# Kernel optimization log

Hardware: AMD Instinct MI355X
Metric: run time of the kernel (lower is better)

Reference implementation:

```python
import jax, jax.numpy as jnp
import numpy as np

V, E, H, L, T_BLOCK = 50257, 1024, 16, 8, 1024
HS = E // H  # 64
F_ = 4 * E
STD = 0.02


def _ln(x, g, b, eps=1e-5):
    mu = jnp.mean(x, axis=-1, keepdims=True)
    var = jnp.var(x, axis=-1, keepdims=True)
    return (x - mu) * jax.lax.rsqrt(var + eps) * g + b


def setup_inputs() -> dict:
    key = jax.random.key(0)
    ks = jax.random.split(key, 16)
    n = lambda k, shp: (STD * jax.random.normal(k, shp)).astype(jnp.float32)
    inp = {
        "idx": jax.random.randint(ks[0], (4, 1024), 0, V, dtype=jnp.int32).astype(jnp.int64),
        "tok_emb": n(ks[1], (V, E)),
        "pos_emb": n(ks[2], (T_BLOCK, E)),
        "wq": n(ks[3], (L, H, E, HS)),
        "wk": n(ks[4], (L, H, E, HS)),
        "wv": n(ks[5], (L, H, E, HS)),
        "wo": n(ks[6], (L, E, E)),
        "bo": jnp.zeros((L, E), jnp.float32),
        "ln1g": jnp.ones((L, E), jnp.float32),
        "ln1b": jnp.zeros((L, E), jnp.float32),
        "ln2g": jnp.ones((L, E), jnp.float32),
        "ln2b": jnp.zeros((L, E), jnp.float32),
        "w1": n(ks[7], (L, E, F_)),
        "b1": jnp.zeros((L, F_), jnp.float32),
        "w2": n(ks[8], (L, F_, E)),
        "b2": jnp.zeros((L, E), jnp.float32),
        "lnfg": jnp.ones((E,), jnp.float32),
        "lnfb": jnp.zeros((E,), jnp.float32),
    }
    return inp


def reference(idx, tok_emb, pos_emb, wq, wk, wv, wo, bo, ln1g, ln1b,
              ln2g, ln2b, w1, b1, w2, b2, lnfg, lnfb):
    B, T = idx.shape
    x = tok_emb[idx] + pos_emb[:T]  # [B,T,E]
    mask = jnp.tril(jnp.ones((T, T), dtype=bool))  # causal
    scale = HS ** -0.5
    for l in range(L):
        h = _ln(x, ln1g[l], ln1b[l])
        q = jnp.einsum('bte,hed->bhtd', h, wq[l])
        k = jnp.einsum('bte,hed->bhtd', h, wk[l])
        v = jnp.einsum('bte,hed->bhtd', h, wv[l])
        att = jnp.einsum('bhtd,bhsd->bhts', q, k) * scale
        att = jnp.where(mask, att, -jnp.inf)
        att = jax.nn.softmax(att, axis=-1)
        o = jnp.einsum('bhts,bhsd->bhtd', att, v)
        o = o.transpose(0, 2, 1, 3).reshape(B, T, E)  # concat heads
        x = x + o @ wo[l] + bo[l]
        h2 = _ln(x, ln2g[l], ln2b[l])
        x = x + jax.nn.relu(h2 @ w1[l] + b1[l]) @ w2[l] + b2[l]
    x = _ln(x, lnfg, lnfb)
    logits = x @ tok_emb.T  # tied lm_head, no bias
    return logits
```

## Files before the change

kernel.cpp:

```cpp
#include <hip/hip_runtime.h>
#include <cstdint>

#define B_ 4
#define T_ 1024
#define E_ 1024
#define H_ 16
#define HS_ 64
#define L_ 8
#define F_DIM 4096
#define V_ 50257
#define VP_ 50304

typedef __attribute__((ext_vector_type(8))) short bf16x8;
typedef __attribute__((ext_vector_type(4))) float f32x4;
typedef unsigned short u16;

__device__ inline float b2f(u16 u) {
  unsigned int v = ((unsigned int)u) << 16;
  return __builtin_bit_cast(float, v);
}
__device__ inline u16 f2b(float f) {
  unsigned int u = __builtin_bit_cast(unsigned int, f);
  unsigned int r = (u + 0x7FFFu + ((u >> 16) & 1u)) >> 16;
  return (u16)r;
}

__device__ inline float wave_sum(float v) {
#pragma unroll
  for (int off = 32; off > 0; off >>= 1) v += __shfl_down(v, off);
  return v;
}

#define GLOAD16(gp, lp)                                                        \
  __builtin_amdgcn_global_load_lds(                                            \
      (const __attribute__((address_space(1))) unsigned int*)(gp),             \
      (__attribute__((address_space(3))) unsigned int*)(lp), 16, 0, 0)

__global__ __launch_bounds__(256) void embed_kernel(
    const int* __restrict__ idx, const float* __restrict__ tok,
    const float* __restrict__ pos, float* __restrict__ x) {
  int bt = blockIdx.x;
  int t = bt & (T_ - 1);
  int tid = threadIdx.x;
  int tokid = idx[bt];
  float4 a = reinterpret_cast<const float4*>(tok + (size_t)tokid * E_)[tid];
  float4 p = reinterpret_cast<const float4*>(pos + (size_t)t * E_)[tid];
  float4 r = make_float4(a.x + p.x, a.y + p.y, a.z + p.z, a.w + p.w);
  reinterpret_cast<float4*>(x + (size_t)bt * E_)[tid] = r;
}

__global__ __launch_bounds__(256) void ln_kernel(
    const float* __restrict__ in, const float* __restrict__ g,
    const float* __restrict__ b, u16* __restrict__ out) {
  int row = blockIdx.x;
  int tid = threadIdx.x;
  const float* xr = in + (size_t)row * E_;
  float4 v = reinterpret_cast<const float4*>(xr)[tid];
  float s = v.x + v.y + v.z + v.w;
  float q = v.x * v.x + v.y * v.y + v.z * v.z + v.w * v.w;
  s = wave_sum(s);
  q = wave_sum(q);
  __shared__ float ls[4], lq[4];
  int wid = tid >> 6;
  if ((tid & 63) == 0) { ls[wid] = s; lq[wid] = q; }
  __syncthreads();
  float st = ls[0] + ls[1] + ls[2] + ls[3];
  float qt = lq[0] + lq[1] + lq[2] + lq[3];
  float mu = st * (1.0f / E_);
  float var = qt * (1.0f / E_) - mu * mu;
  float inv = rsqrtf(var + 1e-5f);
  float4 gg = reinterpret_cast<const float4*>(g)[tid];
  float4 bb = reinterpret_cast<const float4*>(b)[tid];
  ushort4 o4;
  o4.x = f2b((v.x - mu) * inv * gg.x + bb.x);
  o4.y = f2b((v.y - mu) * inv * gg.y + bb.y);
  o4.z = f2b((v.z - mu) * inv * gg.z + bb.z);
  o4.w = f2b((v.w - mu) * inv * gg.w + bb.w);
  reinterpret_cast<ushort4*>(out + (size_t)row * E_)[tid] = o4;
}

__global__ __launch_bounds__(256) void convT_kernel(
    const float* __restrict__ in, u16* __restrict__ out, int K, int N) {
  __shared__ float tile[64][65];
  int n0 = blockIdx.x * 64, k0 = blockIdx.y * 64;
  int tx = threadIdx.x & 63, ty = threadIdx.x >> 6;
#pragma unroll
  for (int r = 0; r < 64; r += 4)
    tile[r + ty][tx] = in[(size_t)(k0 + r + ty) * N + n0 + tx];
  __syncthreads();
#pragma unroll
  for (int r = 0; r < 64; r += 4)
    out[(size_t)(n0 + r + ty) * K + k0 + tx] = f2b(tile[tx][r + ty]);
}

__global__ __launch_bounds__(256) void convQKV_kernel(
    const float* __restrict__ wq, const float* __restrict__ wk,
    const float* __restrict__ wv, u16* __restrict__ out) {
  int src = blockIdx.x >> 4, hh = blockIdx.x & 15, e0 = blockIdx.y * 64;
  const float* w =
      (src == 0 ? wq : (src == 1 ? wk : wv)) + (size_t)hh * E_ * HS_;
  __shared__ float tile[64][65];
  int tx = threadIdx.x & 63, ty = threadIdx.x >> 6;
#pragma unroll
  for (int r = 0; r < 64; r += 4)
    tile[r + ty][tx] = w[(size_t)(e0 + r + ty) * HS_ + tx];
  __syncthreads();
  size_t nb = (size_t)src * 1024 + hh * 64;
#pragma unroll
  for (int r = 0; r < 64; r += 4)
    out[(nb + r + ty) * E_ + e0 + tx] = f2b(tile[tx][r + ty]);
}

__global__ __launch_bounds__(256) void convTok_kernel(
    const float* __restrict__ tok, u16* __restrict__ out) {
  int row = blockIdx.x;
  int tid = threadIdx.x;
  ushort4 o4;
  if (row < V_) {
    float4 v = reinterpret_cast<const float4*>(tok + (size_t)row * E_)[tid];
    o4.x = f2b(v.x); o4.y = f2b(v.y); o4.z = f2b(v.z); o4.w = f2b(v.w);
  } else {
    o4 = make_ushort4(0, 0, 0, 0);
  }
  reinterpret_cast<ushort4*>(out + (size_t)row * E_)[tid] = o4;
}

__global__ __launch_bounds__(256) void vtrans_kernel(
    const u16* __restrict__ qkv, u16* __restrict__ vt) {
  int t0 = blockIdx.x * 64;
  int bh = blockIdx.y;
  int b = bh >> 4, hh = bh & 15;
  __shared__ unsigned int tile[64][65];
  int tx = threadIdx.x & 63, ty = threadIdx.x >> 6;
  const u16* src = qkv + ((size_t)(b * T_ + t0)) * 3072 + 2048 + hh * 64;
#pragma unroll
  for (int r = 0; r < 64; r += 4)
    tile[r + ty][tx] = src[(size_t)(r + ty) * 3072 + tx];
  __syncthreads();
  u16* dst = vt + ((size_t)bh * 64) * 1024 + t0;
#pragma unroll
  for (int r = 0; r < 64; r += 4)
    dst[(size_t)(r + ty) * 1024 + tx] = (u16)tile[tx][r + ty];
}

__global__ __launch_bounds__(256) void mfma_gemm_kernel(
    const u16* __restrict__ A, int lda, const u16* __restrict__ Bt, int ldb,
    const float* __restrict__ bias, float* __restrict__ Cf,
    u16* __restrict__ Cb, int ldc, int N, int K, int flags) {
  __shared__ u16 As[128 * 32];
  __shared__ u16 Bs[128 * 32];
  int m0 = blockIdx.x * 128, n0 = blockIdx.y * 128;
  int tid = threadIdx.x;
  int wave = tid >> 6, lane = tid & 63;
  int wr = wave >> 1, wc = wave & 1;

  f32x4 acc[4][4];
#pragma unroll
  for (int i = 0; i < 4; ++i)
#pragma unroll
    for (int j = 0; j < 4; ++j) acc[i][j] = (f32x4){0.f, 0.f, 0.f, 0.f};

  int c0 = wave * 2, c1 = wave * 2 + 1;
  int sr0 = c0 * 16 + (lane >> 2), sr1 = c1 * 16 + (lane >> 2);
  int sc = (lane & 3) * 8;
  const u16* Ag0 = A + (size_t)(m0 + sr0) * lda + sc;
  const u16* Ag1 = A + (size_t)(m0 + sr1) * lda + sc;
  const u16* Bg0 = Bt + (size_t)(n0 + sr0) * ldb + sc;
  const u16* Bg1 = Bt + (size_t)(n0 + sr1) * ldb + sc;
  u16* lA0 = &As[c0 * 512];
  u16* lA1 = &As[c1 * 512];
  u16* lB0 = &Bs[c0 * 512];
  u16* lB1 = &Bs[c1 * 512];

  int lrow = lane & 15, loct = lane >> 4;
  const int arow0 = (wr * 64 + lrow) * 32 + loct * 8;
  const int brow0 = (wc * 64 + lrow) * 32 + loct * 8;

  for (int k0 = 0; k0 < K; k0 += 32) {
    GLOAD16(Ag0 + k0, lA0);
    GLOAD16(Ag1 + k0, lA1);
    GLOAD16(Bg0 + k0, lB0);
    GLOAD16(Bg1 + k0, lB1);
    __syncthreads();
    bf16x8 af[4], bfr[4];
#pragma unroll
    for (int mf = 0; mf < 4; ++mf)
      af[mf] = *(const bf16x8*)&As[arow0 + mf * 16 * 32];
#pragma unroll
    for (int nf = 0; nf < 4; ++nf)
      bfr[nf] = *(const bf16x8*)&Bs[brow0 + nf * 16 * 32];
#pragma unroll
    for (int mf = 0; mf < 4; ++mf)
#pragma unroll
      for (int nf = 0; nf < 4; ++nf)
        acc[mf][nf] = __builtin_amdgcn_mfma_f32_16x16x32_bf16(
            af[mf], bfr[nf], acc[mf][nf], 0, 0, 0);
    __syncthreads();
  }

  int lq = lane >> 4;
#pragma unroll
  for (int mf = 0; mf < 4; ++mf) {
#pragma unroll
    for (int nf = 0; nf < 4; ++nf) {
      int n = n0 + wc * 64 + nf * 16 + lrow;
      if (n < N) {
        float bv = bias ? bias[n] : 0.f;
#pragma unroll
        for (int j = 0; j < 4; ++j) {
          int m = m0 + wr * 64 + mf * 16 + lq * 4 + j;
          float r = acc[mf][nf][j] + bv;
          if (flags & 1) r += Cf[(size_t)m * ldc + n];
          if (flags & 2) r = fmaxf(r, 0.f);
          if (Cb)
            Cb[(size_t)m * ldc + n] = f2b(r);
          else
            Cf[(size_t)m * ldc + n] = r;
        }
      }
    }
  }
}

__global__ __launch_bounds__(256) void fattn_kernel(
    const u16* __restrict__ qkv, const u16* __restrict__ vt,
    u16* __restrict__ o) {
  int t0 = (gridDim.x - 1 - blockIdx.x) * 64;
  int bh = blockIdx.y;
  int b = bh >> 4, hh = bh & 15;
  int tid = threadIdx.x;
  int w = tid >> 6, lane = tid & 63;
  int c = lane & 15, g = lane >> 4;

  __shared__ u16 Ks[64][72];
  __shared__ u16 Vs[64][72];
  __shared__ u16 Ps[4][16][72];

  const u16* qbase = qkv + (size_t)(b * T_) * 3072 + hh * 64;
  const u16* kbase = qbase + 1024;
  const u16* vbase = vt + (size_t)bh * 64 * 1024;

  bf16x8 qf[2];
  {
    const u16* qrow = qbase + (size_t)(t0 + w * 16 + c) * 3072 + g * 8;
#pragma unroll
    for (int kh = 0; kh < 2; ++kh) {
      bf16x8 tq = *(const bf16x8*)(qrow + kh * 32);
#pragma unroll
      for (int j = 0; j < 8; ++j) tq[j] = (short)f2b(b2f((u16)tq[j]) * 0.125f);
      qf[kh] = tq;
    }
  }

  float m[4] = {-1e30f, -1e30f, -1e30f, -1e30f};
  float l[4] = {0.f, 0.f, 0.f, 0.f};
  f32x4 acc[4];
#pragma unroll
  for (int ds = 0; ds < 4; ++ds) acc[ds] = (f32x4){0.f, 0.f, 0.f, 0.f};

  int tq0 = t0 + w * 16 + g * 4;

  for (int kv0 = 0; kv0 <= t0; kv0 += 64) {
    __syncthreads();
#pragma unroll
    for (int i = tid; i < 512; i += 256) {
      int r = i >> 3, cc = i & 7;
      *(int4*)&Ks[r][cc * 8] =
          *(const int4*)(kbase + (size_t)(kv0 + r) * 3072 + cc * 8);
      *(int4*)&Vs[r][cc * 8] =
          *(const int4*)(vbase + (size_t)r * 1024 + kv0 + cc * 8);
    }
    __syncthreads();

    f32x4 s[4];
#pragma unroll
    for (int ct = 0; ct < 4; ++ct) {
      bf16x8 kf0 = *(const bf16x8*)&Ks[ct * 16 + c][g * 8];
      bf16x8 kf1 = *(const bf16x8*)&Ks[ct * 16 + c][g * 8 + 32];
      s[ct] = (f32x4){0.f, 0.f, 0.f, 0.f};
      s[ct] =
          __builtin_amdgcn_mfma_f32_16x16x32_bf16(qf[0], kf0, s[ct], 0, 0, 0);
      s[ct] =
          __builtin_amdgcn_mfma_f32_16x16x32_bf16(qf[1], kf1, s[ct], 0, 0, 0);
    }
#pragma unroll
    for (int ct = 0; ct < 4; ++ct) {
      int tk = kv0 + ct * 16 + c;
#pragma unroll
      for (int j = 0; j < 4; ++j)
        if (tk > tq0 + j) s[ct][j] = -1e30f;
    }
#pragma unroll
    for (int j = 0; j < 4; ++j) {
      float mt = fmaxf(fmaxf(s[0][j], s[1][j]), fmaxf(s[2][j], s[3][j]));
#pragma unroll
      for (int off = 1; off < 16; off <<= 1)
        mt = fmaxf(mt, __shfl_xor(mt, off));
      float mn = fmaxf(m[j], mt);
      float sc = __expf(m[j] - mn);
      m[j] = mn;
      float rs = 0.f;
#pragma unroll
      for (int ct = 0; ct < 4; ++ct) {
        float p = __expf(s[ct][j] - mn);
        s[ct][j] = p;
        rs += p;
      }
#pragma unroll
      for (int off = 1; off < 16; off <<= 1) rs += __shfl_xor(rs, off);
      l[j] = l[j] * sc + rs;
#pragma unroll
      for (int ds = 0; ds < 4; ++ds) acc[ds][j] *= sc;
    }
#pragma unroll
    for (int ct = 0; ct < 4; ++ct)
#pragma unroll
      for (int j = 0; j < 4; ++j)
        Ps[w][g * 4 + j][ct * 16 + c] = f2b(s[ct][j]);
    bf16x8 pf0 = *(const bf16x8*)&Ps[w][c][g * 8];
    bf16x8 pf1 = *(const bf16x8*)&Ps[w][c][g * 8 + 32];
#pragma unroll
    for (int ds = 0; ds < 4; ++ds) {
      bf16x8 vf0 = *(const bf16x8*)&Vs[ds * 16 + c][g * 8];
      bf16x8 vf1 = *(const bf16x8*)&Vs[ds * 16 + c][g * 8 + 32];
      acc[ds] =
          __builtin_amdgcn_mfma_f32_16x16x32_bf16(pf0, vf0, acc[ds], 0, 0, 0);
      acc[ds] =
          __builtin_amdgcn_mfma_f32_16x16x32_bf16(pf1, vf1, acc[ds], 0, 0, 0);
    }
  }

  float inv[4];
#pragma unroll
  for (int j = 0; j < 4; ++j) inv[j] = 1.0f / l[j];
  u16* orow = o + ((size_t)(b * T_ + tq0)) * E_ + hh * 64;
#pragma unroll
  for (int ds = 0; ds < 4; ++ds)
#pragma unroll
    for (int j = 0; j < 4; ++j)
      orow[(size_t)j * E_ + ds * 16 + c] = f2b(acc[ds][j] * inv[j]);
}

extern "C" void kernel_launch(void* const* d_in, const int* in_sizes, int n_in,
                              void* d_out, int out_size, void* d_ws,
                              size_t ws_size, hipStream_t stream) {
  (void)in_sizes; (void)n_in; (void)out_size; (void)ws_size;
  const int* idx = (const int*)d_in[0];
  const float* tok_emb = (const float*)d_in[1];
  const float* pos_emb = (const float*)d_in[2];
  const float* wq = (const float*)d_in[3];
  const float* wk = (const float*)d_in[4];
  const float* wv = (const float*)d_in[5];
  const float* wo = (const float*)d_in[6];
  const float* bo = (const float*)d_in[7];
  const float* ln1g = (const float*)d_in[8];
  const float* ln1b = (const float*)d_in[9];
  const float* ln2g = (const float*)d_in[10];
  const float* ln2b = (const float*)d_in[11];
  const float* w1 = (const float*)d_in[12];
  const float* b1 = (const float*)d_in[13];
  const float* w2 = (const float*)d_in[14];
  const float* b2 = (const float*)d_in[15];
  const float* lnfg = (const float*)d_in[16];
  const float* lnfb = (const float*)d_in[17];
  float* out = (float*)d_out;
  char* ws = (char*)d_ws;

  u16* h = (u16*)(ws + 0);
  float* x = (float*)(ws + 8388608);
  u16* qkvb = (u16*)(ws + 25165824);
  u16* ob = (u16*)(ws + 50331648);
  u16* ffb = (u16*)(ws + 58720256);
  u16* wqkvT = (u16*)(ws + 92274688);
  u16* woT = (u16*)(ws + 98566144);
  u16* w1T = (u16*)(ws + 100663296);
  u16* w2T = (u16*)(ws + 109051904);
  u16* vtb = (u16*)(ws + 117440512);
  u16* tokb = (u16*)(ws + 8388608);

  embed_kernel<<<B_ * T_, 256, 0, stream>>>(idx, tok_emb, pos_emb, x);

  for (int l = 0; l < L_; ++l) {
    ln_kernel<<<B_ * T_, 256, 0, stream>>>(x, ln1g + l * E_, ln1b + l * E_, h);
    convQKV_kernel<<<dim3(48, 16), 256, 0, stream>>>(
        wq + (size_t)l * H_ * E_ * HS_, wk + (size_t)l * H_ * E_ * HS_,
        wv + (size_t)l * H_ * E_ * HS_, wqkvT);
    mfma_gemm_kernel<<<dim3(32, 24), 256, 0, stream>>>(
        h, E_, wqkvT, E_, nullptr, nullptr, qkvb, 3072, 3072, E_, 0);
    vtrans_kernel<<<dim3(16, 64), 256, 0, stream>>>(qkvb, vtb);
    fattn_kernel<<<dim3(16, 64), 256, 0, stream>>>(qkvb, vtb, ob);
    convT_kernel<<<dim3(16, 16), 256, 0, stream>>>(
        wo + (size_t)l * E_ * E_, woT, E_, E_);
    mfma_gemm_kernel<<<dim3(32, 8), 256, 0, stream>>>(
        ob, E_, woT, E_, bo + (size_t)l * E_, x, nullptr, E_, E_, E_, 1);
    ln_kernel<<<B_ * T_, 256, 0, stream>>>(x, ln2g + l * E_, ln2b + l * E_, h);
    convT_kernel<<<dim3(64, 16), 256, 0, stream>>>(
        w1 + (size_t)l * E_ * F_DIM, w1T, E_, F_DIM);
    mfma_gemm_kernel<<<dim3(32, 32), 256, 0, stream>>>(
        h, E_, w1T, E_, b1 + (size_t)l * F_DIM, nullptr, ffb, F_DIM, F_DIM,
        E_, 2);
    convT_kernel<<<dim3(16, 64), 256, 0, stream>>>(
        w2 + (size_t)l * F_DIM * E_, w2T, F_DIM, E_);
    mfma_gemm_kernel<<<dim3(32, 8), 256, 0, stream>>>(
        ffb, F_DIM, w2T, F_DIM, b2 + (size_t)l * E_, x, nullptr, E_, E_,
        F_DIM, 1);
  }

  ln_kernel<<<B_ * T_, 256, 0, stream>>>(x, lnfg, lnfb, h);
  convTok_kernel<<<VP_, 256, 0, stream>>>(tok_emb, tokb);
  mfma_gemm_kernel<<<dim3(32, VP_ / 128), 256, 0, stream>>>(
      h, E_, tokb, E_, nullptr, out, nullptr, V_, V_, E_, 0);
}
```

Before: 3.641 ms.

## Add 256x256 double-buffered MFMA GEMM with XCD-aware block remap

Adds a new 512-thread GEMM kernel that uses 256x256 output tiles and 64-wide K steps. Operands are staged in double-buffered, XOR-swizzled LDS through direct global-to-LDS loads, and each next-tile prefetch is interleaved with the current tile's MFMA work under explicit waitcnt and barrier control. Workgroup IDs are remapped so consecutive tiles land on the same XCD, which should improve L2 reuse. The QKV, FFN-up and lm_head GEMMs switch to this kernel, with vocab padding raised to a multiple of 256. This raises LDS use to 128KB per block and lowers occupancy, and the convTok workspace now holds more padded rows.

Measured after the change: 3.324 ms. -8.7%, faster.

```diff
diff --git a/kernel.cpp b/kernel.cpp
--- a/kernel.cpp
+++ b/kernel.cpp
@@ -9,7 +9,7 @@
 #define L_ 8
 #define F_DIM 4096
 #define V_ 50257
-#define VP_ 50304
+#define VP2_ 50432
 
 typedef __attribute__((ext_vector_type(8))) short bf16x8;
 typedef __attribute__((ext_vector_type(4))) float f32x4;
@@ -143,6 +143,145 @@
     dst[(size_t)(r + ty) * 1024 + tx] = (u16)tile[tx][r + ty];
 }
 
+__global__ __launch_bounds__(512) void gemm8p_kernel(
+    const u16* __restrict__ A, int lda, const u16* __restrict__ Bt, int ldb,
+    const float* __restrict__ bias, float* __restrict__ Cf,
+    u16* __restrict__ Cb, int ldc, int N, int K, int gn, int flags) {
+  __shared__ u16 As[2][256 * 64];
+  __shared__ u16 Bs[2][256 * 64];
+
+  int nwg = gridDim.x;
+  int q8 = nwg >> 3;
+  int bid = blockIdx.x;
+  int wg = (bid & 7) * q8 + (bid >> 3);
+  int m0 = (wg / gn) * 256, n0 = (wg % gn) * 256;
+
+  int tid = threadIdx.x;
+  int w = tid >> 6, lane = tid & 63;
+  int wr = w >> 2, wc = w & 3;
+  int l15 = lane & 15, lg = lane >> 4;
+  int swzr = (l15 & 7) << 3;
+
+  int l8 = lane >> 3;
+  int swz_e = ((lane & 7) ^ l8) << 3;
+  int wq = w & 3, wh = w >> 2;
+  const u16* aSrc[4];
+  const u16* bSrc[4];
+#pragma unroll
+  for (int qq = 0; qq < 4; ++qq) {
+    aSrc[qq] = A + (size_t)(m0 + wh * 128 + qq * 32 + wq * 8 + l8) * lda;
+    bSrc[qq] = Bt + (size_t)(n0 + (w >> 1) * 64 + qq * 16 + (w & 1) * 8 + l8) * ldb;
+  }
+
+#define STAGE_A(qq, tt, bb)                                                    \
+  GLOAD16(aSrc[qq] + (size_t)(tt) * 64 + swz_e,                                \
+          &As[bb][(wh * 128 + (qq) * 32 + wq * 8) * 64])
+#define STAGE_B(qq, tt, bb)                                                    \
+  GLOAD16(bSrc[qq] + (size_t)(tt) * 64 + swz_e,                                \
+          &Bs[bb][((w >> 1) * 64 + (qq) * 16 + (w & 1) * 8) * 64])
+#define LDA_OFF(mf, ks) \
+  (((wr * 128 + (mf) * 16 + l15) * 64) + ((((ks) * 32) + lg * 8) ^ swzr))
+#define LDB_OFF(nf, ks) \
+  (((wc * 64 + (nf) * 16 + l15) * 64) + ((((ks) * 32) + lg * 8) ^ swzr))
+#define WAITV(n) asm volatile("s_waitcnt vmcnt(" #n ")" ::: "memory")
+
+  f32x4 acc[8][4];
+#pragma unroll
+  for (int i = 0; i < 8; ++i)
+#pragma unroll
+    for (int j = 0; j < 4; ++j) acc[i][j] = (f32x4){0.f, 0.f, 0.f, 0.f};
+
+  STAGE_B(0, 0, 0); STAGE_B(1, 0, 0); STAGE_B(2, 0, 0); STAGE_B(3, 0, 0);
+  STAGE_A(0, 0, 0); STAGE_A(1, 0, 0); STAGE_A(2, 0, 0); STAGE_A(3, 0, 0);
+  WAITV(3);
+  __builtin_amdgcn_sched_barrier(0);
+  __builtin_amdgcn_s_barrier();
+  __builtin_amdgcn_sched_barrier(0);
+
+  int NT = K >> 6;
+  bf16x8 bfrag[4][2];
+  for (int t = 0; t < NT; ++t) {
+    int cur = t & 1, nxt = cur ^ 1;
+    bool pf = (t + 1 < NT);
+    int t1 = t + 1;
+#pragma unroll
+    for (int p = 0; p < 4; ++p) {
+      bf16x8 a0k0 = *(const bf16x8*)&As[cur][LDA_OFF(2 * p + 0, 0)];
+      bf16x8 a0k1 = *(const bf16x8*)&As[cur][LDA_OFF(2 * p + 0, 1)];
+      bf16x8 a1k0 = *(const bf16x8*)&As[cur][LDA_OFF(2 * p + 1, 0)];
+      bf16x8 a1k1 = *(const bf16x8*)&As[cur][LDA_OFF(2 * p + 1, 1)];
+      if (p == 0) {
+#pragma unroll
+        for (int nf = 0; nf < 4; ++nf) {
+          bfrag[nf][0] = *(const bf16x8*)&Bs[cur][LDB_OFF(nf, 0)];
+          bfrag[nf][1] = *(const bf16x8*)&Bs[cur][LDB_OFF(nf, 1)];
+        }
+      }
+      if (pf) {
+        if (p == 0) { STAGE_B(0, t1, nxt); STAGE_B(1, t1, nxt); }
+        else if (p == 1) { STAGE_B(2, t1, nxt); STAGE_B(3, t1, nxt); }
+        else if (p == 2) { STAGE_A(0, t1, nxt); STAGE_A(1, t1, nxt); }
+        else { STAGE_A(2, t1, nxt); STAGE_A(3, t1, nxt); }
+      }
+      __builtin_amdgcn_s_barrier();
+      asm volatile("s_waitcnt lgkmcnt(0)" ::: "memory");
+      __builtin_amdgcn_sched_barrier(0);
+      __builtin_amdgcn_s_setprio(1);
+#pragma unroll
+      for (int nf = 0; nf < 4; ++nf) {
+        acc[2 * p + 0][nf] = __builtin_amdgcn_mfma_f32_16x16x32_bf16(
+            a0k0, bfrag[nf][0], acc[2 * p + 0][nf], 0, 0, 0);
+        acc[2 * p + 0][nf] = __builtin_amdgcn_mfma_f32_16x16x32_bf16(
+            a0k1, bfrag[nf][1], acc[2 * p + 0][nf], 0, 0, 0);
+        acc[2 * p + 1][nf] = __builtin_amdgcn_mfma_f32_16x16x32_bf16(
+            a1k0, bfrag[nf][0], acc[2 * p + 1][nf], 0, 0, 0);
+        acc[2 * p + 1][nf] = __builtin_amdgcn_mfma_f32_16x16x32_bf16(
+            a1k1, bfrag[nf][1], acc[2 * p + 1][nf], 0, 0, 0);
+      }
+      __builtin_amdgcn_s_setprio(0);
+      if (pf) {
+        if (p == 0) WAITV(4);
+        else if (p == 1) WAITV(5);
+        else if (p == 2) WAITV(6);
+        else WAITV(3);
+      } else {
+        if (p == 0) WAITV(2);
+        else if (p == 1) WAITV(1);
+        else WAITV(0);
+      }
+      __builtin_amdgcn_sched_barrier(0);
+      __builtin_amdgcn_s_barrier();
+      __builtin_amdgcn_sched_barrier(0);
+    }
+  }
+
+#pragma unroll
+  for (int mf = 0; mf < 8; ++mf) {
+#pragma unroll
+    for (int nf = 0; nf < 4; ++nf) {
+      int n = n0 + wc * 64 + nf * 16 + l15;
+      if (n < N) {
+        float bv = bias ? bias[n] : 0.f;
+#pragma unroll
+        for (int j = 0; j < 4; ++j) {
+          int m = m0 + wr * 128 + mf * 16 + lg * 4 + j;
+          float r = acc[mf][nf][j] + bv;
+          if (flags & 2) r = fmaxf(r, 0.f);
+          if (Cb)
+            Cb[(size_t)m * ldc + n] = f2b(r);
+          else
+            Cf[(size_t)m * ldc + n] = r;
+        }
+      }
+    }
+  }
+#undef STAGE_A
+#undef STAGE_B
+#undef LDA_OFF
+#undef LDB_OFF
+#undef WAITV
+}
+
 __global__ __launch_bounds__(256) void mfma_gemm_kernel(
     const u16* __restrict__ A, int lda, const u16* __restrict__ Bt, int ldb,
     const float* __restrict__ bias, float* __restrict__ Cf,
@@ -385,8 +524,8 @@
     convQKV_kernel<<<dim3(48, 16), 256, 0, stream>>>(
         wq + (size_t)l * H_ * E_ * HS_, wk + (size_t)l * H_ * E_ * HS_,
         wv + (size_t)l * H_ * E_ * HS_, wqkvT);
-    mfma_gemm_kernel<<<dim3(32, 24), 256, 0, stream>>>(
-        h, E_, wqkvT, E_, nullptr, nullptr, qkvb, 3072, 3072, E_, 0);
+    gemm8p_kernel<<<16 * 12, 512, 0, stream>>>(
+        h, E_, wqkvT, E_, nullptr, nullptr, qkvb, 3072, 3072, E_, 12, 0);
     vtrans_kernel<<<dim3(16, 64), 256, 0, stream>>>(qkvb, vtb);
     fattn_kernel<<<dim3(16, 64), 256, 0, stream>>>(qkvb, vtb, ob);
     convT_kernel<<<dim3(16, 16), 256, 0, stream>>>(
@@ -396,9 +535,9 @@
     ln_kernel<<<B_ * T_, 256, 0, stream>>>(x, ln2g + l * E_, ln2b + l * E_, h);
     convT_kernel<<<dim3(64, 16), 256, 0, stream>>>(
         w1 + (size_t)l * E_ * F_DIM, w1T, E_, F_DIM);
-    mfma_gemm_kernel<<<dim3(32, 32), 256, 0, stream>>>(
+    gemm8p_kernel<<<16 * 16, 512, 0, stream>>>(
         h, E_, w1T, E_, b1 + (size_t)l * F_DIM, nullptr, ffb, F_DIM, F_DIM,
-        E_, 2);
+        E_, 16, 2);
     convT_kernel<<<dim3(16, 64), 256, 0, stream>>>(
         w2 + (size_t)l * F_DIM * E_, w2T, F_DIM, E_);
     mfma_gemm_kernel<<<dim3(32, 8), 256, 0, stream>>>(
@@ -407,7 +546,7 @@
   }
 
   ln_kernel<<<B_ * T_, 256, 0, stream>>>(x, lnfg, lnfb, h);
-  convTok_kernel<<<VP_, 256, 0, stream>>>(tok_emb, tokb);
-  mfma_gemm_kernel<<<dim3(32, VP_ / 128), 256, 0, stream>>>(
-      h, E_, tokb, E_, nullptr, out, nullptr, V_, V_, E_, 0);
-}
+  convTok_kernel<<<VP2_, 256, 0, stream>>>(tok_emb, tokb);
+  gemm8p_kernel<<<16 * (VP2_ / 256), 512, 0, stream>>>(
+      h, E_, tokb, E_, nullptr, out, nullptr, V_, V_, E_, VP2_ / 256, 0);
+}
```
